# Performance work log

Measured on AMD Instinct MI355X. Metric: run time of the kernel, lower is better.

## Reference

```python
import jax, jax.numpy as jnp
import numpy as np

# Config from VoVNetBEVTransformer: D=41, C=128, downsample=16, final_dim=(128,352)
B, N, C = 4, 6, 128
D, FH, FW = 41, 8, 22
OGH, OGW = 128, 352
XB = (-50.0, 50.0, 0.5)
YB = (-50.0, 50.0, 0.5)
ZB = (-10.0, 10.0, 20.0)
DBOUND = (4.0, 45.0, 1.0)
NX = int((XB[1] - XB[0]) / XB[2])  # 200
NY = int((YB[1] - YB[0]) / YB[2])  # 200
NZ = int((ZB[1] - ZB[0]) / ZB[2])  # 1


def _grid():
    dx = jnp.array([XB[2], YB[2], ZB[2]], jnp.float32)
    bx = jnp.array([XB[0] + XB[2] / 2.0, YB[0] + YB[2] / 2.0, ZB[0] + ZB[2] / 2.0], jnp.float32)
    return dx, bx


def _frustum():
    # (D, FH, FW, 3) grid of (u_pixel, v_pixel, depth) as in create_frustum
    ds = jnp.arange(DBOUND[0], DBOUND[1], DBOUND[2], dtype=jnp.float32)
    xs = jnp.linspace(0.0, OGW - 1.0, FW, dtype=jnp.float32)
    ys = jnp.linspace(0.0, OGH - 1.0, FH, dtype=jnp.float32)
    ds = jnp.broadcast_to(ds[:, None, None], (D, FH, FW))
    xs = jnp.broadcast_to(xs[None, None, :], (D, FH, FW))
    ys = jnp.broadcast_to(ys[None, :, None], (D, FH, FW))
    return jnp.stack([xs, ys, ds], axis=-1)


def setup_inputs() -> dict:
    key = jax.random.key(0)
    ks = jax.random.split(key, 6)
    cam_feats = jax.random.normal(ks[0], (B, N, D, FH, FW, C), jnp.float32)
    # cam-to-ego rotation: camera z (forward) -> ego x, plus small perturbation
    Rbase = jnp.array([[0.0, 0.0, 1.0], [-1.0, 0.0, 0.0], [0.0, -1.0, 0.0]], jnp.float32)
    rots = Rbase[None, None] + 0.02 * jax.random.normal(ks[1], (B, N, 3, 3), jnp.float32)
    trans = 1.5 * jax.random.normal(ks[2], (B, N, 3), jnp.float32)
    K = jnp.array([[500.0, 0.0, 176.0], [0.0, 500.0, 64.0], [0.0, 0.0, 1.0]], jnp.float32)
    intrins = K[None, None] + 0.5 * jax.random.normal(ks[3], (B, N, 3, 3), jnp.float32)
    post_rots = jnp.eye(3, dtype=jnp.float32)[None, None] + 0.01 * jax.random.normal(ks[4], (B, N, 3, 3), jnp.float32)
    post_trans = 0.5 * jax.random.normal(ks[5], (B, N, 3), jnp.float32)
    return {"cam_feats": cam_feats, "rots": rots, "trans": trans, "intrins": intrins,
            "post_rots": post_rots, "post_trans": post_trans}


def reference(cam_feats, rots, trans, intrins, post_rots, post_trans):
    dx, bx = _grid()
    frustum = _frustum()  # (D,FH,FW,3)
    # --- get_geometry ---
    pts = frustum[None, None] - post_trans[:, :, None, None, None, :]          # (B,N,D,FH,FW,3)
    pts = jnp.einsum('bnij,bndhwj->bndhwi', jnp.linalg.inv(post_rots), pts)
    pts = jnp.concatenate([pts[..., :2] * pts[..., 2:3], pts[..., 2:3]], axis=-1)
    combine = rots @ jnp.linalg.inv(intrins)
    pts = jnp.einsum('bnij,bndhwj->bndhwi', combine, pts) + trans[:, :, None, None, None, :]
    # --- voxel_pooling (QuickCumsum == segment-sum over voxel ranks) ---
    x = cam_feats.reshape(-1, C)                                               # (Nprime, C)
    g = ((pts - (bx - dx / 2.0)) / dx).astype(jnp.int32).reshape(-1, 3)        # trunc like torch .long()
    b_ix = jnp.repeat(jnp.arange(B, dtype=jnp.int32), N * D * FH * FW)
    kept = ((g[:, 0] >= 0) & (g[:, 0] < NX) & (g[:, 1] >= 0) & (g[:, 1] < NY)
            & (g[:, 2] >= 0) & (g[:, 2] < NZ))
    gc = jnp.clip(g, 0, jnp.array([NX - 1, NY - 1, NZ - 1], jnp.int32))
    S = NX * NY * NZ * B
    seg = ((gc[:, 0] * NY + gc[:, 1]) * NZ + gc[:, 2]) * B + b_ix              # same rank formula
    seg = jnp.where(kept, seg, S)                                              # dummy bin for dropped pts
    pooled = jax.ops.segment_sum(x, seg, num_segments=S + 1)[:S]               # (S, C)
    final = pooled.reshape(NX, NY, NZ, B, C).transpose(3, 2, 4, 0, 1)          # (B,NZ,C,NX,NY)
    return final.reshape(B, NZ * C, NX, NY)                                    # cat along z -> channels
```

## Files before the change

### kernel.cpp

```cpp
#include <hip/hip_runtime.h>

#define BATCH 4
#define NCAM  6
#define DNUM  41
#define FHN   8
#define FWN   22
#define CCH   128
#define NXV   200
#define NYV   200
#define NXY   40000
#define NPTS  173184
#define SBINS (BATCH * NXY)
#define CAP   64
#define OVF_MAX 8192

struct Mats {
    float iR[9];
    float comb[9];
    float tr[3];
    float pt[3];
};

__device__ void inv3x3_f32_gesv(const float* __restrict__ Ain, float* __restrict__ inv) {
#pragma clang fp contract(off)
    float A[9];
    for (int k = 0; k < 9; ++k) A[k] = Ain[k];
    int piv[3];
    for (int j = 0; j < 3; ++j) {
        int p = j;
        float amax = fabsf(A[j * 3 + j]);
        for (int i = j + 1; i < 3; ++i) {
            float v = fabsf(A[i * 3 + j]);
            if (v > amax) { amax = v; p = i; }
        }
        piv[j] = p;
        if (p != j)
            for (int k = 0; k < 3; ++k) { float t = A[j*3+k]; A[j*3+k] = A[p*3+k]; A[p*3+k] = t; }
        float rd = 1.0f / A[j * 3 + j];
        for (int i = j + 1; i < 3; ++i) A[i * 3 + j] = A[i * 3 + j] * rd;
        for (int i = j + 1; i < 3; ++i)
            for (int k = j + 1; k < 3; ++k)
                A[i * 3 + k] = A[i * 3 + k] - A[i * 3 + j] * A[j * 3 + k];
    }
    float rdiag[3] = {1.0f / A[0], 1.0f / A[4], 1.0f / A[8]};
    for (int c = 0; c < 3; ++c) {
        float b[3] = {0.0f, 0.0f, 0.0f};
        b[c] = 1.0f;
        for (int j = 0; j < 3; ++j) { int p = piv[j]; if (p != j) { float t = b[j]; b[j] = b[p]; b[p] = t; } }
        for (int k = 0; k < 3; ++k)
            for (int i = k + 1; i < 3; ++i)
                b[i] = b[i] - A[i * 3 + k] * b[k];
        for (int k = 2; k >= 0; --k) {
            b[k] = b[k] * rdiag[k];
            for (int i = 0; i < k; ++i)
                b[i] = b[i] - A[i * 3 + k] * b[k];
        }
        inv[0 + c] = b[0];
        inv[3 + c] = b[1];
        inv[6 + c] = b[2];
    }
}

__global__ void prep_kernel(const float* __restrict__ rots,
                            const float* __restrict__ trans,
                            const float* __restrict__ intrins,
                            const float* __restrict__ post_rots,
                            const float* __restrict__ post_trans,
                            Mats* __restrict__ mats) {
    int i = threadIdx.x;
    if (i >= BATCH * NCAM) return;
    Mats m;
    inv3x3_f32_gesv(post_rots + i * 9, m.iR);
    float invK[9];
    inv3x3_f32_gesv(intrins + i * 9, invK);
    {
#pragma clang fp contract(off)
        for (int r = 0; r < 3; ++r)
            for (int c = 0; c < 3; ++c) {
                float s = rots[i * 9 + r * 3 + 0] * invK[0 * 3 + c];
                s = s + rots[i * 9 + r * 3 + 1] * invK[1 * 3 + c];
                s = s + rots[i * 9 + r * 3 + 2] * invK[2 * 3 + c];
                m.comb[r * 3 + c] = s;
            }
    }
    for (int k = 0; k < 3; ++k) {
        m.tr[k] = trans[i * 3 + k];
        m.pt[k] = post_trans[i * 3 + k];
    }
    mats[i] = m;
}

__device__ __forceinline__ int point_voxel(int p, const Mats* __restrict__ mats) {
#pragma clang fp contract(off)
    int w = p % FWN;
    int t = p / FWN;
    int h = t % FHN;
    t /= FHN;
    int d = t % DNUM;
    t /= DNUM;
    int n = t % NCAM;
    int b = t / NCAM;

    const Mats m = mats[b * NCAM + n];

    float u   = (float)((double)w * (351.0 / 21.0));
    float v   = (float)((double)h * (127.0 / 7.0));
    float dep = 4.0f + (float)d;

    float p0 = u - m.pt[0];
    float p1 = v - m.pt[1];
    float p2 = dep - m.pt[2];
    float q0 = m.iR[0] * p0; q0 = q0 + m.iR[1] * p1; q0 = q0 + m.iR[2] * p2;
    float q1 = m.iR[3] * p0; q1 = q1 + m.iR[4] * p1; q1 = q1 + m.iR[5] * p2;
    float q2 = m.iR[6] * p0; q2 = q2 + m.iR[7] * p1; q2 = q2 + m.iR[8] * p2;
    float r0 = q0 * q2;
    float r1 = q1 * q2;
    float e0 = m.comb[0] * r0; e0 = e0 + m.comb[1] * r1; e0 = e0 + m.comb[2] * q2; e0 = e0 + m.tr[0];
    float e1 = m.comb[3] * r0; e1 = e1 + m.comb[4] * r1; e1 = e1 + m.comb[5] * q2; e1 = e1 + m.tr[1];
    float e2 = m.comb[6] * r0; e2 = e2 + m.comb[7] * r1; e2 = e2 + m.comb[8] * q2; e2 = e2 + m.tr[2];

    float gxf = (e0 + 50.0f) / 0.5f;
    float gyf = (e1 + 50.0f) / 0.5f;
    float gzf = (e2 + 10.0f) / 20.0f;
    int gx = (int)gxf;
    int gy = (int)gyf;
    int gz = (int)gzf;
    if (gx < 0 || gx >= NXV || gy < 0 || gy >= NYV || gz < 0 || gz >= 1) return -1;
    return b * NXY + gx * NYV + gy;
}


__global__ __launch_bounds__(256) void bucket_kernel(const Mats* __restrict__ mats,
                                                     int* __restrict__ counts,
                                                     int* __restrict__ bucket,
                                                     int* __restrict__ ovfcnt,
                                                     int2* __restrict__ ovf) {
    int p = blockIdx.x * 256 + threadIdx.x;
    if (p >= NPTS) return;
    int vid = point_voxel(p, mats);
    if (vid < 0) return;
    int slot = atomicAdd(&counts[vid], 1);
    if (slot < CAP) {
        bucket[(size_t)vid * CAP + slot] = p;
    } else {
        int o = atomicAdd(ovfcnt, 1);
        if (o < OVF_MAX) ovf[o] = make_int2(vid, p);
    }
}

__global__ __launch_bounds__(256) void gather3_kernel(const float* __restrict__ feats,
                                                      const int* __restrict__ counts,
                                                      const int* __restrict__ bucket,
                                                      const int* __restrict__ ovfcnt,
                                                      const int2* __restrict__ ovf,
                                                      float* __restrict__ out) {
    __shared__ float acc[32][129];
    int t = threadIdx.x;
    int j = t >> 3;
    int g = t & 7;
    int xy0 = blockIdx.x * 32;
    int b = blockIdx.y;
    int bin = b * NXY + xy0 + j;

    int cntRaw = counts[bin];
    int cnt = cntRaw < CAP ? cntRaw : CAP;

    float4 a0 = {0.f,0.f,0.f,0.f}, a1 = a0, a2 = a0, a3 = a0;
    const int* bk = bucket + (size_t)bin * CAP;
    const float* fg = feats + g * 16;

    int k = 0;
    for (; k + 4 <= cnt; k += 4) {
        int4 pp = *(const int4*)(bk + k);
        const float4* f0 = (const float4*)(fg + (size_t)pp.x * CCH);
        const float4* f1 = (const float4*)(fg + (size_t)pp.y * CCH);
        const float4* f2 = (const float4*)(fg + (size_t)pp.z * CCH);
        const float4* f3 = (const float4*)(fg + (size_t)pp.w * CCH);
        float4 v00 = f0[0], v01 = f0[1], v02 = f0[2], v03 = f0[3];
        float4 v10 = f1[0], v11 = f1[1], v12 = f1[2], v13 = f1[3];
        float4 v20 = f2[0], v21 = f2[1], v22 = f2[2], v23 = f2[3];
        float4 v30 = f3[0], v31 = f3[1], v32 = f3[2], v33 = f3[3];
        a0.x += v00.x; a0.y += v00.y; a0.z += v00.z; a0.w += v00.w;
        a1.x += v01.x; a1.y += v01.y; a1.z += v01.z; a1.w += v01.w;
        a2.x += v02.x; a2.y += v02.y; a2.z += v02.z; a2.w += v02.w;
        a3.x += v03.x; a3.y += v03.y; a3.z += v03.z; a3.w += v03.w;
        a0.x += v10.x; a0.y += v10.y; a0.z += v10.z; a0.w += v10.w;
        a1.x += v11.x; a1.y += v11.y; a1.z += v11.z; a1.w += v11.w;
        a2.x += v12.x; a2.y += v12.y; a2.z += v12.z; a2.w += v12.w;
        a3.x += v13.x; a3.y += v13.y; a3.z += v13.z; a3.w += v13.w;
        a0.x += v20.x; a0.y += v20.y; a0.z += v20.z; a0.w += v20.w;
        a1.x += v21.x; a1.y += v21.y; a1.z += v21.z; a1.w += v21.w;
        a2.x += v22.x; a2.y += v22.y; a2.z += v22.z; a2.w += v22.w;
        a3.x += v23.x; a3.y += v23.y; a3.z += v23.z; a3.w += v23.w;
        a0.x += v30.x; a0.y += v30.y; a0.z += v30.z; a0.w += v30.w;
        a1.x += v31.x; a1.y += v31.y; a1.z += v31.z; a1.w += v31.w;
        a2.x += v32.x; a2.y += v32.y; a2.z += v32.z; a2.w += v32.w;
        a3.x += v33.x; a3.y += v33.y; a3.z += v33.z; a3.w += v33.w;
    }
    for (; k < cnt; ++k) {
        int p = bk[k];
        const float4* f4 = (const float4*)(fg + (size_t)p * CCH);
        float4 v0 = f4[0], v1 = f4[1], v2 = f4[2], v3 = f4[3];
        a0.x += v0.x; a0.y += v0.y; a0.z += v0.z; a0.w += v0.w;
        a1.x += v1.x; a1.y += v1.y; a1.z += v1.z; a1.w += v1.w;
        a2.x += v2.x; a2.y += v2.y; a2.z += v2.z; a2.w += v2.w;
        a3.x += v3.x; a3.y += v3.y; a3.z += v3.z; a3.w += v3.w;
    }

    int novf = ovfcnt[0];
    if (novf > 0) {
        if (novf > OVF_MAX) novf = OVF_MAX;
        for (int e = 0; e < novf; ++e) {
            int2 vp = ovf[e];
            if (vp.x == bin) {
                const float4* f4 = (const float4*)(fg + (size_t)vp.y * CCH);
                float4 v0 = f4[0], v1 = f4[1], v2 = f4[2], v3 = f4[3];
                a0.x += v0.x; a0.y += v0.y; a0.z += v0.z; a0.w += v0.w;
                a1.x += v1.x; a1.y += v1.y; a1.z += v1.z; a1.w += v1.w;
                a2.x += v2.x; a2.y += v2.y; a2.z += v2.z; a2.w += v2.w;
                a3.x += v3.x; a3.y += v3.y; a3.z += v3.z; a3.w += v3.w;
            }
        }
    }

    int nz = __syncthreads_count(cnt != 0);
    int tx = t & 31, tg = t >> 5;
    float* dst = out + (size_t)b * CCH * NXY + xy0 + tx;
    if (nz == 0) {
#pragma unroll
        for (int cc = 0; cc < 16; ++cc)
            dst[(size_t)(cc * 8 + tg) * NXY] = 0.0f;
        return;
    }

    float* row = &acc[j][g * 16];
    row[0]  = a0.x; row[1]  = a0.y; row[2]  = a0.z; row[3]  = a0.w;
    row[4]  = a1.x; row[5]  = a1.y; row[6]  = a1.z; row[7]  = a1.w;
    row[8]  = a2.x; row[9]  = a2.y; row[10] = a2.z; row[11] = a2.w;
    row[12] = a3.x; row[13] = a3.y; row[14] = a3.z; row[15] = a3.w;
    __syncthreads();

#pragma unroll
    for (int cc = 0; cc < 16; ++cc) {
        int ch = cc * 8 + tg;
        dst[(size_t)ch * NXY] = acc[tx][ch];
    }
}

__global__ __launch_bounds__(128) void scatter_direct_kernel(const float* __restrict__ feats,
                                                             const Mats* __restrict__ mats,
                                                             float* __restrict__ out) {
    int p = blockIdx.x;
    int vid = point_voxel(p, mats);
    if (vid < 0) return;
    int b  = vid / NXY;
    int xy = vid % NXY;
    int c = threadIdx.x;
    float f = feats[(size_t)p * CCH + c];
    atomicAdd(out + (size_t)(b * CCH + c) * NXY + xy, f);
}

extern "C" void kernel_launch(void* const* d_in, const int* in_sizes, int n_in,
                              void* d_out, int out_size, void* d_ws, size_t ws_size,
                              hipStream_t stream) {
    const float* cam_feats  = (const float*)d_in[0];
    const float* rots       = (const float*)d_in[1];
    const float* trans      = (const float*)d_in[2];
    const float* intrins    = (const float*)d_in[3];
    const float* post_rots  = (const float*)d_in[4];
    const float* post_trans = (const float*)d_in[5];
    float* out = (float*)d_out;
    Mats* mats = (Mats*)d_ws;

    const size_t OFF_COUNTS = 4096;
    const size_t OFF_OVFCNT = OFF_COUNTS + (size_t)SBINS * 4;
    const size_t OFF_OVF    = OFF_OVFCNT + 256;
    const size_t OFF_BUCKET = OFF_OVF + (size_t)OVF_MAX * 8;
    const size_t WS_NEEDED  = OFF_BUCKET + (size_t)SBINS * CAP * 4;

    prep_kernel<<<1, 64, 0, stream>>>(rots, trans, intrins, post_rots, post_trans, mats);

    if (ws_size >= WS_NEEDED) {
        int*  counts = (int*)((char*)d_ws + OFF_COUNTS);
        int*  ovfcnt = (int*)((char*)d_ws + OFF_OVFCNT);
        int2* ovf    = (int2*)((char*)d_ws + OFF_OVF);
        int*  bucket = (int*)((char*)d_ws + OFF_BUCKET);

        hipMemsetAsync(counts, 0, (size_t)SBINS * 4 + 256, stream);

        const int ptBlocks = (NPTS + 255) / 256;
        bucket_kernel<<<ptBlocks, 256, 0, stream>>>(mats, counts, bucket, ovfcnt, ovf);

        dim3 ggrid(NXY / 32, BATCH);
        gather3_kernel<<<ggrid, 256, 0, stream>>>(cam_feats, counts, bucket, ovfcnt, ovf, out);
    } else {
        hipMemsetAsync(d_out, 0, (size_t)out_size * sizeof(float), stream);
        scatter_direct_kernel<<<NPTS, CCH, 0, stream>>>(cam_feats, mats, out);
    }
}
```

Baseline: 229.2 us.

## Fuse matrix prep into bucket kernel and stage bucket indices in shared memory

Removes the separate prep_kernel launch by recomputing the per-camera matrices inside every bucket_kernel block and keeping them in shared memory, with the 3x3 inversion rewritten in unrolled register form. The gather kernel now cooperatively loads bin counts and the first eight bucket indices per bin into shared memory before the feature loop, so the index loads are issued together rather than serialized before each feature fetch. The cost is redundant matrix computation in every block, plus an extra barrier and shared memory in the gather kernel.

```diff
diff --git a/kernel.cpp b/kernel.cpp
--- a/kernel.cpp
+++ b/kernel.cpp
@@ -13,6 +13,7 @@
 #define SBINS (BATCH * NXY)
 #define CAP   64
 #define OVF_MAX 8192
+#define NSTAGE 8
 
 struct Mats {
     float iR[9];
@@ -21,43 +22,77 @@
     float pt[3];
 };
 
-__device__ void inv3x3_f32_gesv(const float* __restrict__ Ain, float* __restrict__ inv) {
+__device__ __forceinline__ void inv3x3_f32_gesv_reg(const float* __restrict__ Ain,
+                                                    float* __restrict__ inv) {
 #pragma clang fp contract(off)
-    float A[9];
-    for (int k = 0; k < 9; ++k) A[k] = Ain[k];
-    int piv[3];
-    for (int j = 0; j < 3; ++j) {
-        int p = j;
-        float amax = fabsf(A[j * 3 + j]);
-        for (int i = j + 1; i < 3; ++i) {
-            float v = fabsf(A[i * 3 + j]);
-            if (v > amax) { amax = v; p = i; }
-        }
-        piv[j] = p;
-        if (p != j)
-            for (int k = 0; k < 3; ++k) { float t = A[j*3+k]; A[j*3+k] = A[p*3+k]; A[p*3+k] = t; }
-        float rd = 1.0f / A[j * 3 + j];
-        for (int i = j + 1; i < 3; ++i) A[i * 3 + j] = A[i * 3 + j] * rd;
-        for (int i = j + 1; i < 3; ++i)
-            for (int k = j + 1; k < 3; ++k)
-                A[i * 3 + k] = A[i * 3 + k] - A[i * 3 + j] * A[j * 3 + k];
-    }
-    float rdiag[3] = {1.0f / A[0], 1.0f / A[4], 1.0f / A[8]};
+    float a00=Ain[0], a01=Ain[1], a02=Ain[2];
+    float a10=Ain[3], a11=Ain[4], a12=Ain[5];
+    float a20=Ain[6], a21=Ain[7], a22=Ain[8];
+    int p0, p1;
+    {
+        float amax = fabsf(a00); p0 = 0;
+        float v1 = fabsf(a10); if (v1 > amax) { amax = v1; p0 = 1; }
+        float v2 = fabsf(a20); if (v2 > amax) { p0 = 2; }
+        if (p0 == 1)      { float t; t=a00;a00=a10;a10=t; t=a01;a01=a11;a11=t; t=a02;a02=a12;a12=t; }
+        else if (p0 == 2) { float t; t=a00;a00=a20;a20=t; t=a01;a01=a21;a21=t; t=a02;a02=a22;a22=t; }
+        float rd = 1.0f / a00;
+        a10 = a10 * rd; a20 = a20 * rd;
+        a11 = a11 - a10 * a01; a12 = a12 - a10 * a02;
+        a21 = a21 - a20 * a01; a22 = a22 - a20 * a02;
+    }
+    {
+        float amax = fabsf(a11); p1 = 1;
+        float v2 = fabsf(a21); if (v2 > amax) { p1 = 2; }
+        if (p1 == 2) { float t; t=a10;a10=a20;a20=t; t=a11;a11=a21;a21=t; t=a12;a12=a22;a22=t; }
+        float rd = 1.0f / a11;
+        a21 = a21 * rd;
+        a22 = a22 - a21 * a12;
+    }
+    float rd0 = 1.0f / a00, rd1 = 1.0f / a11, rd2 = 1.0f / a22;
+#pragma unroll
     for (int c = 0; c < 3; ++c) {
-        float b[3] = {0.0f, 0.0f, 0.0f};
-        b[c] = 1.0f;
-        for (int j = 0; j < 3; ++j) { int p = piv[j]; if (p != j) { float t = b[j]; b[j] = b[p]; b[p] = t; } }
-        for (int k = 0; k < 3; ++k)
-            for (int i = k + 1; i < 3; ++i)
-                b[i] = b[i] - A[i * 3 + k] * b[k];
-        for (int k = 2; k >= 0; --k) {
-            b[k] = b[k] * rdiag[k];
-            for (int i = 0; i < k; ++i)
-                b[i] = b[i] - A[i * 3 + k] * b[k];
-        }
-        inv[0 + c] = b[0];
-        inv[3 + c] = b[1];
-        inv[6 + c] = b[2];
+        float b0 = (c==0)?1.0f:0.0f, b1 = (c==1)?1.0f:0.0f, b2 = (c==2)?1.0f:0.0f;
+        if (p0 == 1)      { float t=b0; b0=b1; b1=t; }
+        else if (p0 == 2) { float t=b0; b0=b2; b2=t; }
+        if (p1 == 2)      { float t=b1; b1=b2; b2=t; }
+        b1 = b1 - a10 * b0;
+        b2 = b2 - a20 * b0;
+        b2 = b2 - a21 * b1;
+        b2 = b2 * rd2;
+        b0 = b0 - a02 * b2;
+        b1 = b1 - a12 * b2;
+        b1 = b1 * rd1;
+        b0 = b0 - a01 * b1;
+        b0 = b0 * rd0;
+        inv[0 + c] = b0; inv[3 + c] = b1; inv[6 + c] = b2;
+    }
+}
+
+__device__ __forceinline__ void compute_mats_reg(int i,
+                                                 const float* __restrict__ rots,
+                                                 const float* __restrict__ trans,
+                                                 const float* __restrict__ intrins,
+                                                 const float* __restrict__ post_rots,
+                                                 const float* __restrict__ post_trans,
+                                                 Mats* __restrict__ m) {
+    inv3x3_f32_gesv_reg(post_rots + i * 9, m->iR);
+    float invK[9];
+    inv3x3_f32_gesv_reg(intrins + i * 9, invK);
+    {
+#pragma clang fp contract(off)
+#pragma unroll
+        for (int r = 0; r < 3; ++r)
+#pragma unroll
+            for (int c = 0; c < 3; ++c) {
+                float s = rots[i * 9 + r * 3 + 0] * invK[0 * 3 + c];
+                s = s + rots[i * 9 + r * 3 + 1] * invK[1 * 3 + c];
+                s = s + rots[i * 9 + r * 3 + 2] * invK[2 * 3 + c];
+                m->comb[r * 3 + c] = s;
+            }
+    }
+    for (int k = 0; k < 3; ++k) {
+        m->tr[k] = trans[i * 3 + k];
+        m->pt[k] = post_trans[i * 3 + k];
     }
 }
 
@@ -70,23 +105,7 @@
     int i = threadIdx.x;
     if (i >= BATCH * NCAM) return;
     Mats m;
-    inv3x3_f32_gesv(post_rots + i * 9, m.iR);
-    float invK[9];
-    inv3x3_f32_gesv(intrins + i * 9, invK);
-    {
-#pragma clang fp contract(off)
-        for (int r = 0; r < 3; ++r)
-            for (int c = 0; c < 3; ++c) {
-                float s = rots[i * 9 + r * 3 + 0] * invK[0 * 3 + c];
-                s = s + rots[i * 9 + r * 3 + 1] * invK[1 * 3 + c];
-                s = s + rots[i * 9 + r * 3 + 2] * invK[2 * 3 + c];
-                m.comb[r * 3 + c] = s;
-            }
-    }
-    for (int k = 0; k < 3; ++k) {
-        m.tr[k] = trans[i * 3 + k];
-        m.pt[k] = post_trans[i * 3 + k];
-    }
+    compute_mats_reg(i, rots, trans, intrins, post_rots, post_trans, &m);
     mats[i] = m;
 }
 
@@ -130,46 +149,106 @@
 }
 
 
-__global__ __launch_bounds__(256) void bucket_kernel(const Mats* __restrict__ mats,
+__global__ __launch_bounds__(256) void bucket_kernel(const float* __restrict__ rots,
+                                                     const float* __restrict__ trans,
+                                                     const float* __restrict__ intrins,
+                                                     const float* __restrict__ post_rots,
+                                                     const float* __restrict__ post_trans,
                                                      int* __restrict__ counts,
                                                      int* __restrict__ bucket,
                                                      int* __restrict__ ovfcnt,
                                                      int2* __restrict__ ovf) {
-    int p = blockIdx.x * 256 + threadIdx.x;
-    if (p >= NPTS) return;
-    int vid = point_voxel(p, mats);
-    if (vid < 0) return;
-    int slot = atomicAdd(&counts[vid], 1);
-    if (slot < CAP) {
-        bucket[(size_t)vid * CAP + slot] = p;
-    } else {
-        int o = atomicAdd(ovfcnt, 1);
-        if (o < OVF_MAX) ovf[o] = make_int2(vid, p);
-    }
-}
-
-__global__ __launch_bounds__(256) void gather3_kernel(const float* __restrict__ feats,
+    __shared__ Mats smats[BATCH * NCAM];
+    int t = threadIdx.x;
+    if (t < BATCH * NCAM) {
+        Mats m;
+        compute_mats_reg(t, rots, trans, intrins, post_rots, post_trans, &m);
+        smats[t] = m;
+    }
+    __syncthreads();
+    int p = blockIdx.x * 256 + t;
+    if (p < NPTS) {
+        int vid = point_voxel(p, smats);
+        if (vid >= 0) {
+            int slot = atomicAdd(&counts[vid], 1);
+            if (slot < CAP) {
+                bucket[(size_t)vid * CAP + slot] = p;
+            } else {
+                int o = atomicAdd(ovfcnt, 1);
+                if (o < OVF_MAX) ovf[o] = make_int2(vid, p);
+            }
+        }
+    }
+}
+
+__global__ __launch_bounds__(256) void gather5_kernel(const float* __restrict__ feats,
                                                       const int* __restrict__ counts,
                                                       const int* __restrict__ bucket,
                                                       const int* __restrict__ ovfcnt,
                                                       const int2* __restrict__ ovf,
                                                       float* __restrict__ out) {
     __shared__ float acc[32][129];
+    __shared__ int s_idx[32][9];
+    __shared__ int s_cnt[32];
     int t = threadIdx.x;
     int j = t >> 3;
     int g = t & 7;
     int xy0 = blockIdx.x * 32;
     int b = blockIdx.y;
-    int bin = b * NXY + xy0 + j;
-
-    int cntRaw = counts[bin];
+    int bin0 = b * NXY + xy0;
+    int bin = bin0 + j;
+
+    int novf = ovfcnt[0];
+
+    if (t < 32) s_cnt[t] = counts[bin0 + t];
+    s_idx[j][g] = bucket[(size_t)bin * CAP + g];
+    __syncthreads();
+
+    int cntRaw = s_cnt[j];
     int cnt = cntRaw < CAP ? cntRaw : CAP;
 
     float4 a0 = {0.f,0.f,0.f,0.f}, a1 = a0, a2 = a0, a3 = a0;
+    const float* fg = feats + g * 16;
     const int* bk = bucket + (size_t)bin * CAP;
-    const float* fg = feats + g * 16;
-
+
+    int kmax8 = cnt < NSTAGE ? cnt : NSTAGE;
     int k = 0;
+    for (; k + 4 <= kmax8; k += 4) {
+        int pp0 = s_idx[j][k], pp1 = s_idx[j][k+1], pp2 = s_idx[j][k+2], pp3 = s_idx[j][k+3];
+        const float4* f0 = (const float4*)(fg + (size_t)pp0 * CCH);
+        const float4* f1 = (const float4*)(fg + (size_t)pp1 * CCH);
+        const float4* f2 = (const float4*)(fg + (size_t)pp2 * CCH);
+        const float4* f3 = (const float4*)(fg + (size_t)pp3 * CCH);
+        float4 v00 = f0[0], v01 = f0[1], v02 = f0[2], v03 = f0[3];
+        float4 v10 = f1[0], v11 = f1[1], v12 = f1[2], v13 = f1[3];
+        float4 v20 = f2[0], v21 = f2[1], v22 = f2[2], v23 = f2[3];
+        float4 v30 = f3[0], v31 = f3[1], v32 = f3[2], v33 = f3[3];
+        a0.x += v00.x; a0.y += v00.y; a0.z += v00.z; a0.w += v00.w;
+        a1.x += v01.x; a1.y += v01.y; a1.z += v01.z; a1.w += v01.w;
+        a2.x += v02.x; a2.y += v02.y; a2.z += v02.z; a2.w += v02.w;
+        a3.x += v03.x; a3.y += v03.y; a3.z += v03.z; a3.w += v03.w;
+        a0.x += v10.x; a0.y += v10.y; a0.z += v10.z; a0.w += v10.w;
+        a1.x += v11.x; a1.y += v11.y; a1.z += v11.z; a1.w += v11.w;
+        a2.x += v12.x; a2.y += v12.y; a2.z += v12.z; a2.w += v12.w;
+        a3.x += v13.x; a3.y += v13.y; a3.z += v13.z; a3.w += v13.w;
+        a0.x += v20.x; a0.y += v20.y; a0.z += v20.z; a0.w += v20.w;
+        a1.x += v21.x; a1.y += v21.y; a1.z += v21.z; a1.w += v21.w;
+        a2.x += v22.x; a2.y += v22.y; a2.z += v22.z; a2.w += v22.w;
+        a3.x += v23.x; a3.y += v23.y; a3.z += v23.z; a3.w += v23.w;
+        a0.x += v30.x; a0.y += v30.y; a0.z += v30.z; a0.w += v30.w;
+        a1.x += v31.x; a1.y += v31.y; a1.z += v31.z; a1.w += v31.w;
+        a2.x += v32.x; a2.y += v32.y; a2.z += v32.z; a2.w += v32.w;
+        a3.x += v33.x; a3.y += v33.y; a3.z += v33.z; a3.w += v33.w;
+    }
+    for (; k < kmax8; ++k) {
+        int p = s_idx[j][k];
+        const float4* f4 = (const float4*)(fg + (size_t)p * CCH);
+        float4 v0 = f4[0], v1 = f4[1], v2 = f4[2], v3 = f4[3];
+        a0.x += v0.x; a0.y += v0.y; a0.z += v0.z; a0.w += v0.w;
+        a1.x += v1.x; a1.y += v1.y; a1.z += v1.z; a1.w += v1.w;
+        a2.x += v2.x; a2.y += v2.y; a2.z += v2.z; a2.w += v2.w;
+        a3.x += v3.x; a3.y += v3.y; a3.z += v3.z; a3.w += v3.w;
+    }
     for (; k + 4 <= cnt; k += 4) {
         int4 pp = *(const int4*)(bk + k);
         const float4* f0 = (const float4*)(fg + (size_t)pp.x * CCH);
@@ -207,7 +286,6 @@
         a3.x += v3.x; a3.y += v3.y; a3.z += v3.z; a3.w += v3.w;
     }
 
-    int novf = ovfcnt[0];
     if (novf > 0) {
         if (novf > OVF_MAX) novf = OVF_MAX;
         for (int e = 0; e < novf; ++e) {
@@ -270,7 +348,6 @@
     const float* post_rots  = (const float*)d_in[4];
     const float* post_trans = (const float*)d_in[5];
     float* out = (float*)d_out;
-    Mats* mats = (Mats*)d_ws;
 
     const size_t OFF_COUNTS = 4096;
     const size_t OFF_OVFCNT = OFF_COUNTS + (size_t)SBINS * 4;
@@ -278,8 +355,6 @@
     const size_t OFF_BUCKET = OFF_OVF + (size_t)OVF_MAX * 8;
     const size_t WS_NEEDED  = OFF_BUCKET + (size_t)SBINS * CAP * 4;
 
-    prep_kernel<<<1, 64, 0, stream>>>(rots, trans, intrins, post_rots, post_trans, mats);
-
     if (ws_size >= WS_NEEDED) {
         int*  counts = (int*)((char*)d_ws + OFF_COUNTS);
         int*  ovfcnt = (int*)((char*)d_ws + OFF_OVFCNT);
@@ -289,11 +364,14 @@
         hipMemsetAsync(counts, 0, (size_t)SBINS * 4 + 256, stream);
 
         const int ptBlocks = (NPTS + 255) / 256;
-        bucket_kernel<<<ptBlocks, 256, 0, stream>>>(mats, counts, bucket, ovfcnt, ovf);
+        bucket_kernel<<<ptBlocks, 256, 0, stream>>>(rots, trans, intrins, post_rots,
+                                                    post_trans, counts, bucket, ovfcnt, ovf);
 
         dim3 ggrid(NXY / 32, BATCH);
-        gather3_kernel<<<ggrid, 256, 0, stream>>>(cam_feats, counts, bucket, ovfcnt, ovf, out);
+        gather5_kernel<<<ggrid, 256, 0, stream>>>(cam_feats, counts, bucket, ovfcnt, ovf, out);
     } else {
+        Mats* mats = (Mats*)d_ws;
+        prep_kernel<<<1, 64, 0, stream>>>(rots, trans, intrins, post_rots, post_trans, mats);
         hipMemsetAsync(d_out, 0, (size_t)out_size * sizeof(float), stream);
         scatter_direct_kernel<<<NPTS, CCH, 0, stream>>>(cam_feats, mats, out);
     }
```

Result: no change. 231.4 us (+0.9%).
